# Kernel optimization log

Hardware: AMD Instinct MI355X
Metric: run time of the kernel (lower is better)

The kernel has to match this reference:

```python
import jax, jax.numpy as jnp
import numpy as np

HIDDEN = 1024
N_EMB = 4096
K_TOP = 64
EPS = 1e-6


def rmsnorm(x, w):
    xf = x.astype(jnp.float32)
    y = xf * jax.lax.rsqrt(jnp.mean(xf * xf, axis=-1, keepdims=True) + EPS)
    return y.astype(x.dtype) * w


def setup_inputs() -> dict:
    key = jax.random.key(0)
    ks = jax.random.split(key, 5)
    B, S, D, N = 16, 2048, HIDDEN, N_EMB
    bound = 1.0 / np.sqrt(D)  # torch Linear reset_parameters uniform bound
    return {
        "X": jax.random.normal(ks[0], (B, S, D), dtype=jnp.float32),
        "alpha": jnp.zeros((), dtype=jnp.float32),
        "E": jax.random.normal(ks[1], (N, D), dtype=jnp.float32) / np.sqrt(D),
        "Wq": jax.random.uniform(ks[2], (D, D), dtype=jnp.float32, minval=-bound, maxval=bound),
        "Wk": jax.random.uniform(ks[3], (D, D), dtype=jnp.float32, minval=-bound, maxval=bound),
        "xn_w": jnp.ones((D,), dtype=jnp.float32),
        "sn_w": jnp.ones((D,), dtype=jnp.float32),
        "on_w": jnp.ones((D,), dtype=jnp.float32),
    }


def reference(X, alpha, E, Wq, Wk, xn_w, sn_w, on_w):
    scale = HIDDEN ** (-0.5)
    Xn = rmsnorm(X, xn_w)            # (B,S,D)
    En = rmsnorm(E, sn_w)            # (N,D)
    Q = Xn @ Wq.T                    # (B,S,D)
    Km = En @ Wk.T                   # (N,D)
    scores = jnp.einsum('bsd,nd->bsn', Q, Km) * scale  # (B,S,N)
    global_scores = jnp.max(scores, axis=1)            # (B,N)
    top_vals, _ = jax.lax.top_k(global_scores, K_TOP)
    cutoff = top_vals[:, -1:]                          # (B,1)
    masked = jnp.where(global_scores >= cutoff, global_scores, -jnp.inf)
    dense_w = jax.nn.softmax(global_scores, axis=-1)
    sparse_w = jax.nn.softmax(masked, axis=-1)
    weights = alpha * dense_w + (1.0 - alpha) * sparse_w  # (B,N)
    O = rmsnorm(weights @ En, on_w)                      # (B,D)
    return O, weights
```

## Files before the change

### kernel.cpp

```cpp
#include <hip/hip_runtime.h>


namespace {

constexpr int D_DIM = 1024;
constexpr int NE    = 4096;
constexpr int BATCH = 16;
constexpr int SEQ   = 2048;
constexpr int MX    = BATCH * SEQ;
constexpr int KTOP  = 64;
constexpr int CAND  = 128;
constexpr int BK    = 32;

using f32x4  = __attribute__((ext_vector_type(4))) float;
using bf16x8 = __attribute__((ext_vector_type(8))) short;
using i32x4  = __attribute__((ext_vector_type(4))) int;

__device__ inline unsigned encf(float f) {
  unsigned u = __float_as_uint(f);
  return (u & 0x80000000u) ? ~u : (u | 0x80000000u);
}
__device__ inline float decf(unsigned e) {
  unsigned u = (e & 0x80000000u) ? (e ^ 0x80000000u) : ~e;
  return __uint_as_float(u);
}

__device__ inline unsigned short f2bf(float f) {
  unsigned u = __float_as_uint(f);
  unsigned lsb = (u >> 16) & 1u;
  u += 0x7fffu + lsb;
  return (unsigned short)(u >> 16);
}
__device__ inline float bf2f(unsigned short h) {
  return __uint_as_float(((unsigned)h) << 16);
}

__device__ inline void gload16(const void* gsrc, void* ldst) {
  __builtin_amdgcn_global_load_lds(
      (const __attribute__((address_space(1))) unsigned int*)gsrc,
      (__attribute__((address_space(3))) unsigned int*)ldst, 16, 0, 0);
}

#define LGK0_SB() do { asm volatile("s_waitcnt lgkmcnt(0)" ::: "memory"); \
                       __builtin_amdgcn_sched_barrier(0); } while (0)

__global__ void row_rinv_k(const float* __restrict__ X, float* __restrict__ rinv) {
  __shared__ float l4[4];
  int row = blockIdx.x;
  float4 v = ((const float4*)(X + (size_t)row * D_DIM))[threadIdx.x];
  float ss = v.x * v.x + v.y * v.y + v.z * v.z + v.w * v.w;
  for (int o = 32; o > 0; o >>= 1) ss += __shfl_xor(ss, o);
  int lane = threadIdx.x & 63, w = threadIdx.x >> 6;
  if (lane == 0) l4[w] = ss;
  __syncthreads();
  if (threadIdx.x == 0) {
    float t = l4[0] + l4[1] + l4[2] + l4[3];
    rinv[row] = rsqrtf(t * (1.0f / D_DIM) + 1e-6f);
  }
}

__global__ void rinv_quantx_k(const float* __restrict__ X, float* __restrict__ rinv,
                              float* __restrict__ sxr, int* __restrict__ XQ) {
  __shared__ float l4[4], m4[4];
  int row = blockIdx.x;
  float4 v = ((const float4*)(X + (size_t)row * D_DIM))[threadIdx.x];
  float ss = v.x * v.x + v.y * v.y + v.z * v.z + v.w * v.w;
  float am = fmaxf(fmaxf(fabsf(v.x), fabsf(v.y)), fmaxf(fabsf(v.z), fabsf(v.w)));
  for (int o = 32; o > 0; o >>= 1) {
    ss += __shfl_xor(ss, o);
    am = fmaxf(am, __shfl_xor(am, o));
  }
  int lane = threadIdx.x & 63, w = threadIdx.x >> 6;
  if (lane == 0) { l4[w] = ss; m4[w] = am; }
  __syncthreads();
  float t  = l4[0] + l4[1] + l4[2] + l4[3];
  float amax = fmaxf(fmaxf(m4[0], m4[1]), fmaxf(m4[2], m4[3]));
  amax = fmaxf(amax, 1e-30f);
  float ri = rsqrtf(t * (1.0f / D_DIM) + 1e-6f);
  if (threadIdx.x == 0) {
    rinv[row] = ri;
    sxr[row]  = ri * amax * (1.0f / 127.0f);
  }
  float qs = 127.0f / amax;
  int q0 = (int)rintf(v.x * qs) & 0xff;
  int q1 = (int)rintf(v.y * qs) & 0xff;
  int q2 = (int)rintf(v.z * qs) & 0xff;
  int q3 = (int)rintf(v.w * qs) & 0xff;
  XQ[(size_t)row * 256 + threadIdx.x] = q0 | (q1 << 8) | (q2 << 16) | (q3 << 24);
}

__global__ void quant_p_k(const unsigned short* __restrict__ PH,
                          const unsigned short* __restrict__ PL,
                          float* __restrict__ sp, int* __restrict__ PQ) {
  __shared__ float m4[4];
  int row = blockIdx.x;
  ushort4 h = *(const ushort4*)(PH + (size_t)row * D_DIM + threadIdx.x * 4);
  ushort4 l = *(const ushort4*)(PL + (size_t)row * D_DIM + threadIdx.x * 4);
  float p0 = bf2f(h.x) + bf2f(l.x);
  float p1 = bf2f(h.y) + bf2f(l.y);
  float p2 = bf2f(h.z) + bf2f(l.z);
  float p3 = bf2f(h.w) + bf2f(l.w);
  float am = fmaxf(fmaxf(fabsf(p0), fabsf(p1)), fmaxf(fabsf(p2), fabsf(p3)));
  for (int o = 32; o > 0; o >>= 1) am = fmaxf(am, __shfl_xor(am, o));
  int lane = threadIdx.x & 63, w = threadIdx.x >> 6;
  if (lane == 0) m4[w] = am;
  __syncthreads();
  float amax = fmaxf(fmaxf(m4[0], m4[1]), fmaxf(m4[2], m4[3]));
  amax = fmaxf(amax, 1e-30f);
  if (threadIdx.x == 0) sp[row] = amax * (1.0f / 127.0f);
  float qs = 127.0f / amax;
  int q0 = (int)rintf(p0 * qs) & 0xff;
  int q1 = (int)rintf(p1 * qs) & 0xff;
  int q2 = (int)rintf(p2 * qs) & 0xff;
  int q3 = (int)rintf(p3 * qs) & 0xff;
  PQ[(size_t)row * 256 + threadIdx.x] = q0 | (q1 << 8) | (q2 << 16) | (q3 << 24);
}

__global__ void prep_w_k(const float* __restrict__ Wq, const float* __restrict__ Wk,
                         const float* __restrict__ cw, float* __restrict__ T,
                         unsigned short* __restrict__ H, unsigned short* __restrict__ L) {
  __shared__ float t[32][33], u[32][33];
  int k0 = blockIdx.x * 32, d0 = blockIdx.y * 32;
  int tx = threadIdx.x & 31, ty4 = (threadIdx.x >> 5) * 4;
#pragma unroll
  for (int i = 0; i < 4; ++i) {
    t[ty4 + i][tx] = Wq[(size_t)(d0 + ty4 + i) * D_DIM + k0 + tx];
    u[ty4 + i][tx] = Wk[(size_t)(d0 + ty4 + i) * D_DIM + k0 + tx];
  }
  __syncthreads();
#pragma unroll
  for (int i = 0; i < 4; ++i) {
    int a = ty4 + i;
    T[(size_t)(k0 + a) * D_DIM + d0 + tx] = t[tx][a];
    float v = u[tx][a] * cw[k0 + a];
    unsigned short h = f2bf(v);
    H[(size_t)(k0 + a) * D_DIM + d0 + tx] = h;
    L[(size_t)(k0 + a) * D_DIM + d0 + tx] = f2bf(v - bf2f(h));
  }
}

template <int FPOUT>
__global__ __launch_bounds__(256, 2) void gemm_a32_k(
    const float* __restrict__ A, const float* __restrict__ rinv,
    const unsigned short* __restrict__ BH, const unsigned short* __restrict__ BL,
    unsigned short* __restrict__ OH, unsigned short* __restrict__ OL,
    float* __restrict__ Of) {
  __shared__ __align__(16) float lA[128 * 32];
  __shared__ __align__(16) unsigned short lBH[128 * 32];
  __shared__ __align__(16) unsigned short lBL[128 * 32];
  __shared__ float ldsR[128];

  int tid = threadIdx.x;
  int lane = tid & 63, wid = tid >> 6;
  int wr = wid >> 1, wc = wid & 1;
  int fr = lane & 15, fg = lane >> 4;
  long m0 = (long)blockIdx.x * 128;
  long n0 = (long)blockIdx.y * 128;

  if (tid < 128) ldsR[tid] = rinv ? rinv[m0 + tid] : 1.0f;

  f32x4 acc[4][4] = {};

  for (int kk = 0; kk < D_DIM; kk += BK) {
#pragma unroll
    for (int i = 0; i < 4; ++i) {
      int chunk = i * 256 + tid;
      int r = chunk >> 3, c = chunk & 7;
      int cs = c ^ (r & 7);
      const float* src = A + (m0 + r) * (long)D_DIM + kk + cs * 4;
      gload16(src, (void*)(lA + ((i * 256 + (tid & ~63)) << 2)));
    }
#pragma unroll
    for (int i = 0; i < 2; ++i) {
      int chunk = i * 256 + tid;
      int r = chunk >> 2, c = chunk & 3;
      int cs = c ^ ((r >> 1) & 3);
      long boff = (n0 + r) * (long)D_DIM + kk + cs * 8;
      int lo = (i * 256 + (tid & ~63)) << 3;
      gload16(BH + boff, (void*)(lBH + lo));
      gload16(BL + boff, (void*)(lBL + lo));
    }
    __syncthreads();

    bf16x8 aH[4], aL[4], bH[4], bL[4];
#pragma unroll
    for (int m = 0; m < 4; ++m) {
      int row = wr * 64 + m * 16 + fr;
      int rm = row & 7;
      f32x4 p0 = *(const f32x4*)(lA + row * 32 + (((fg * 2 + 0) ^ rm) * 4));
      f32x4 p1 = *(const f32x4*)(lA + row * 32 + (((fg * 2 + 1) ^ rm) * 4));
#pragma unroll
      for (int e = 0; e < 8; ++e) {
        float f = (e < 4) ? p0[e] : p1[e - 4];
        unsigned short h = f2bf(f);
        aH[m][e] = (short)h;
        aL[m][e] = (short)f2bf(f - bf2f(h));
      }
    }
#pragma unroll
    for (int n = 0; n < 4; ++n) {
      int row = wc * 64 + n * 16 + fr;
      int sc = fg ^ ((row >> 1) & 3);
      bH[n] = *(const bf16x8*)(lBH + row * 32 + sc * 8);
      bL[n] = *(const bf16x8*)(lBL + row * 32 + sc * 8);
    }
#pragma unroll
    for (int m = 0; m < 4; ++m)
#pragma unroll
      for (int n = 0; n < 4; ++n) {
        acc[m][n] = __builtin_amdgcn_mfma_f32_16x16x32_bf16(aH[m], bH[n], acc[m][n], 0, 0, 0);
        acc[m][n] = __builtin_amdgcn_mfma_f32_16x16x32_bf16(aH[m], bL[n], acc[m][n], 0, 0, 0);
        acc[m][n] = __builtin_amdgcn_mfma_f32_16x16x32_bf16(aL[m], bH[n], acc[m][n], 0, 0, 0);
      }
    __syncthreads();
  }

#pragma unroll
  for (int m = 0; m < 4; ++m) {
#pragma unroll
    for (int j = 0; j < 4; ++j) {
      int rloc = wr * 64 + m * 16 + fg * 4 + j;
      float rv = ldsR[rloc];
      long grow = m0 + rloc;
#pragma unroll
      for (int n = 0; n < 4; ++n) {
        long gcol = n0 + wc * 64 + n * 16 + fr;
        float v = acc[m][n][j] * rv;
        if (FPOUT) {
          Of[grow * D_DIM + gcol] = v;
        } else {
          unsigned short h = f2bf(v);
          OH[grow * D_DIM + gcol] = h;
          OL[grow * D_DIM + gcol] = f2bf(v - bf2f(h));
        }
      }
    }
  }
}

__global__ __launch_bounds__(512, 2) void gemm_scores1_k(
    const signed char* __restrict__ XQ, const signed char* __restrict__ PQ,
    const float* __restrict__ sxr, const float* __restrict__ sp,
    unsigned* __restrict__ gmax) {
  __shared__ __align__(16) signed char lA[2][256 * 64];
  __shared__ __align__(16) signed char lB[2][256 * 64];

  int tid = threadIdx.x;
  int lane = tid & 63, wid = tid >> 6;
  int wr = wid >> 2;
  int wcn = wid & 3;
  int fr = lane & 15, fg = lane >> 4;

  int id = blockIdx.x;
  int xcd = id & 7;
  int r = id >> 3;
  int tile_n = (r & 7) | ((r >> 7) << 3);
  int tile_m = xcd * 16 + ((r >> 3) & 15);
  long m0 = (long)tile_m * 256;
  long n0 = (long)tile_n * 256;

  auto stageTile = [&](int buf, int kt) {
    int kk = kt * 64;
#pragma unroll
    for (int i = 0; i < 2; ++i) {
      int chunk = i * 512 + tid;
      int r2 = chunk >> 2, c = chunk & 3;
      int cs = c ^ ((r2 >> 1) & 3);
      gload16(XQ + (m0 + r2) * (long)D_DIM + kk + cs * 16,
              (void*)(&lA[buf][0] + ((i * 512 + (tid & ~63)) << 4)));
    }
#pragma unroll
    for (int i = 0; i < 2; ++i) {
      int chunk = i * 512 + tid;
      int r2 = chunk >> 2, c = chunk & 3;
      int cs = c ^ ((r2 >> 1) & 3);
      gload16(PQ + (n0 + r2) * (long)D_DIM + kk + cs * 16,
              (void*)(&lB[buf][0] + ((i * 512 + (tid & ~63)) << 4)));
    }
  };

  i32x4 acc[8][4] = {};

  stageTile(0, 0);
  stageTile(1, 1);

  i32x4 aF[4], bF[4];

  for (int kt = 0; kt < 16; ++kt) {
    int cur = kt & 1;
    const signed char* As = &lA[cur][0];
    const signed char* Bs = &lB[cur][0];

    if (kt < 15) {
      asm volatile("s_waitcnt vmcnt(4)" ::: "memory");
    } else {
      asm volatile("s_waitcnt vmcnt(0)" ::: "memory");
    }
    __builtin_amdgcn_s_barrier();

#pragma unroll
    for (int mi = 0; mi < 4; ++mi) {
      int row = wr * 128 + mi * 16 + fr;
      int ck = fg ^ ((row >> 1) & 3);
      aF[mi] = *(const i32x4*)(As + row * 64 + ck * 16);
    }
#pragma unroll
    for (int ni = 0; ni < 2; ++ni) {
      int row = wcn * 64 + ni * 16 + fr;
      int ck = fg ^ ((row >> 1) & 3);
      bF[ni] = *(const i32x4*)(Bs + row * 64 + ck * 16);
    }
    LGK0_SB();
    __builtin_amdgcn_s_setprio(1);
#pragma unroll
    for (int mi = 0; mi < 4; ++mi)
#pragma unroll
      for (int ni = 0; ni < 2; ++ni)
        acc[mi][ni] = __builtin_amdgcn_mfma_i32_16x16x64_i8(
            aF[mi], bF[ni], acc[mi][ni], 0, 0, 0);
    __builtin_amdgcn_s_setprio(0);

#pragma unroll
    for (int ni = 2; ni < 4; ++ni) {
      int row = wcn * 64 + ni * 16 + fr;
      int ck = fg ^ ((row >> 1) & 3);
      bF[ni] = *(const i32x4*)(Bs + row * 64 + ck * 16);
    }
    LGK0_SB();
    __builtin_amdgcn_s_setprio(1);
#pragma unroll
    for (int mi = 0; mi < 4; ++mi)
#pragma unroll
      for (int ni = 2; ni < 4; ++ni)
        acc[mi][ni] = __builtin_amdgcn_mfma_i32_16x16x64_i8(
            aF[mi], bF[ni], acc[mi][ni], 0, 0, 0);
    __builtin_amdgcn_s_setprio(0);

#pragma unroll
    for (int mi = 0; mi < 4; ++mi) {
      int row = wr * 128 + (mi + 4) * 16 + fr;
      int ck = fg ^ ((row >> 1) & 3);
      aF[mi] = *(const i32x4*)(As + row * 64 + ck * 16);
    }
    LGK0_SB();
    __builtin_amdgcn_s_barrier();
    if (kt + 2 < 16) stageTile(cur, kt + 2);
    __builtin_amdgcn_s_setprio(1);
#pragma unroll
    for (int mi = 0; mi < 4; ++mi)
#pragma unroll
      for (int ni = 2; ni < 4; ++ni)
        acc[mi + 4][ni] = __builtin_amdgcn_mfma_i32_16x16x64_i8(
            aF[mi], bF[ni], acc[mi + 4][ni], 0, 0, 0);
    __builtin_amdgcn_s_setprio(0);

    __builtin_amdgcn_s_setprio(1);
#pragma unroll
    for (int mi = 0; mi < 4; ++mi)
#pragma unroll
      for (int ni = 0; ni < 2; ++ni)
        acc[mi + 4][ni] = __builtin_amdgcn_mfma_i32_16x16x64_i8(
            aF[mi], bF[ni], acc[mi + 4][ni], 0, 0, 0);
    __builtin_amdgcn_s_setprio(0);
  }

  int b = (int)(m0 >> 11);
#pragma unroll
  for (int ni = 0; ni < 4; ++ni) {
    long col = n0 + wcn * 64 + ni * 16 + fr;
    float spc = sp[col];
    float v = -3.0e38f;
#pragma unroll
    for (int mi = 0; mi < 8; ++mi) {
      const float* sr = sxr + m0 + wr * 128 + mi * 16 + fg * 4;
#pragma unroll
      for (int j = 0; j < 4; ++j)
        v = fmaxf(v, (float)acc[mi][ni][j] * sr[j]);
    }
    v *= spc;
    v = fmaxf(v, __shfl_xor(v, 16));
    v = fmaxf(v, __shfl_xor(v, 32));
    if (fg == 0) {
      atomicMax(&gmax[(long)b * NE + col], encf(v * 0.03125f));
    }
  }
}

__global__ void cand_select_k(const unsigned* __restrict__ gmax,
                              int* __restrict__ candIdx, unsigned* __restrict__ gmax2) {
  __shared__ unsigned enc[NE];
  __shared__ int ic[257];
  int tid = threadIdx.x;
  int lane = tid & 63, w = tid >> 6;
  int zb = blockIdx.x;
  if (tid < CAND) gmax2[zb * CAND + tid] = 0u;
  const unsigned* g = gmax + (size_t)zb * NE;
  for (int i = tid; i < NE; i += 256) enc[i] = g[i];
  __syncthreads();

  unsigned cur = 0;
  for (int bit = 31; bit >= 0; --bit) {
    unsigned cand = cur | (1u << bit);
    int c = 0;
    for (int i = tid; i < NE; i += 256) c += (enc[i] >= cand) ? 1 : 0;
    for (int o = 32; o > 0; o >>= 1) c += __shfl_xor(c, o);
    __syncthreads();
    if (lane == 0) ic[w] = c;
    __syncthreads();
    int tot = ic[0] + ic[1] + ic[2] + ic[3];
    if (tot >= CAND) cur = cand;
  }

  int myc = 0;
  for (int i = tid; i < NE; i += 256) myc += (enc[i] >= cur) ? 1 : 0;
  __syncthreads();
  ic[tid] = myc;
  __syncthreads();
  if (tid == 0) {
    int s = 0;
    for (int t = 0; t < 256; ++t) { int v = ic[t]; ic[t] = s; s += v; }
  }
  __syncthreads();
  int off = ic[tid];
  for (int i = tid; i < NE; i += 256)
    if (enc[i] >= cur) {
      if (off < CAND) candIdx[zb * CAND + off] = i;
      ++off;
    }
}

__global__ __launch_bounds__(256, 2) void gemm_rescore_k(
    const float* __restrict__ X, const float* __restrict__ rinvA,
    const unsigned short* __restrict__ PH, const unsigned short* __restrict__ PL,
    const int* __restrict__ candIdx, unsigned* __restrict__ gmax2) {
  __shared__ __align__(16) float lA[128 * 32];
  __shared__ __align__(16) unsigned short lBH[128 * 32], lBL[128 * 32];
  __shared__ float ldsR[128];

  int tid = threadIdx.x;
  int lane = tid & 63, wid = tid >> 6;
  int wr = wid >> 1, wc = wid & 1;
  int fr = lane & 15, fg = lane >> 4;
  int z = blockIdx.z;
  long m0 = (long)blockIdx.x * 128;
  long arow0 = (long)z * SEQ + m0;

  if (tid < 128) ldsR[tid] = rinvA[arow0 + tid];

  long bbase[2];
#pragma unroll
  for (int i = 0; i < 2; ++i) {
    int r = (i * 256 + tid) >> 2;
    bbase[i] = (long)candIdx[z * CAND + r] * D_DIM;
  }

  f32x4 acc[4][4] = {};

  for (int kk = 0; kk < D_DIM; kk += BK) {
#pragma unroll
    for (int i = 0; i < 4; ++i) {
      int chunk = i * 256 + tid;
      int r = chunk >> 3, c = chunk & 7;
      int cs = c ^ (r & 7);
      const float* src = X + (arow0 + r) * (long)D_DIM + kk + cs * 4;
      gload16(src, (void*)(lA + ((i * 256 + (tid & ~63)) << 2)));
    }
#pragma unroll
    for (int i = 0; i < 2; ++i) {
      int chunk = i * 256 + tid;
      int c = chunk & 3;
      int r = chunk >> 2;
      int cs = c ^ ((r >> 1) & 3);
      long boff = bbase[i] + kk + cs * 8;
      int lo = (i * 256 + (tid & ~63)) << 3;
      gload16(PH + boff, (void*)(lBH + lo));
      gload16(PL + boff, (void*)(lBL + lo));
    }
    __syncthreads();

    bf16x8 aH[4], aL[4], bH[4], bL[4];
#pragma unroll
    for (int m = 0; m < 4; ++m) {
      int row = wr * 64 + m * 16 + fr;
      int rm = row & 7;
      f32x4 p0 = *(const f32x4*)(lA + row * 32 + (((fg * 2 + 0) ^ rm) * 4));
      f32x4 p1 = *(const f32x4*)(lA + row * 32 + (((fg * 2 + 1) ^ rm) * 4));
#pragma unroll
      for (int e = 0; e < 8; ++e) {
        float f = (e < 4) ? p0[e] : p1[e - 4];
        unsigned short h = f2bf(f);
        aH[m][e] = (short)h;
        aL[m][e] = (short)f2bf(f - bf2f(h));
      }
    }
#pragma unroll
    for (int n = 0; n < 4; ++n) {
      int row = wc * 64 + n * 16 + fr;
      int sc = fg ^ ((row >> 1) & 3);
      bH[n] = *(const bf16x8*)(lBH + row * 32 + sc * 8);
      bL[n] = *(const bf16x8*)(lBL + row * 32 + sc * 8);
    }
#pragma unroll
    for (int m = 0; m < 4; ++m)
#pragma unroll
      for (int n = 0; n < 4; ++n) {
        acc[m][n] = __builtin_amdgcn_mfma_f32_16x16x32_bf16(aH[m], bH[n], acc[m][n], 0, 0, 0);
        acc[m][n] = __builtin_amdgcn_mfma_f32_16x16x32_bf16(aH[m], bL[n], acc[m][n], 0, 0, 0);
        acc[m][n] = __builtin_amdgcn_mfma_f32_16x16x32_bf16(aL[m], bH[n], acc[m][n], 0, 0, 0);
      }
    __syncthreads();
  }

#pragma unroll
  for (int n = 0; n < 4; ++n) {
    float v = -3.0e38f;
#pragma unroll
    for (int m = 0; m < 4; ++m)
#pragma unroll
      for (int j = 0; j < 4; ++j) {
        float rv = ldsR[wr * 64 + m * 16 + fg * 4 + j];
        v = fmaxf(v, acc[m][n][j] * rv);
      }
    v = fmaxf(v, __shfl_xor(v, 16));
    v = fmaxf(v, __shfl_xor(v, 32));
    if (fg == 0) {
      int col = wc * 64 + n * 16 + fr;
      atomicMax(&gmax2[z * CAND + col], encf(v * 0.03125f));
    }
  }
}

__global__ void final_k(const unsigned* __restrict__ gmax,
                        const unsigned* __restrict__ gmax2,
                        const int* __restrict__ candIdx,
                        const float* __restrict__ alpha_p,
                        const float* __restrict__ E, const float* __restrict__ rinvE,
                        const float* __restrict__ sn_w, const float* __restrict__ on_w,
                        float* __restrict__ wout, float* __restrict__ O) {
  __shared__ unsigned enc[NE];
  __shared__ int sel[NE];
  __shared__ unsigned ubc[4];
  __shared__ float l4[4];
  __shared__ int ic[257];
  int tid = threadIdx.x;
  int lane = tid & 63, w = tid >> 6;
  int b = blockIdx.x;
  const unsigned* g = gmax + (size_t)b * NE;
  for (int i = tid; i < NE; i += 256) enc[i] = g[i];
  __syncthreads();
  if (tid < CAND) enc[candIdx[b * CAND + tid]] = gmax2[b * CAND + tid];
  __syncthreads();

  unsigned mx = 0;
  for (int i = tid; i < NE; i += 256) mx = enc[i] > mx ? enc[i] : mx;
  for (int o = 32; o > 0; o >>= 1) {
    unsigned other = (unsigned)__shfl_xor((int)mx, o);
    if (other > mx) mx = other;
  }
  if (lane == 0) ubc[w] = mx;
  __syncthreads();
  unsigned m1e = ubc[0];
  for (int t = 1; t < 4; ++t) m1e = ubc[t] > m1e ? ubc[t] : m1e;
  float m1 = decf(m1e);

  unsigned cur = 0;
  for (int bit = 31; bit >= 0; --bit) {
    unsigned cand = cur | (1u << bit);
    int c = 0;
    for (int i = tid; i < NE; i += 256) c += (enc[i] >= cand) ? 1 : 0;
    for (int o = 32; o > 0; o >>= 1) c += __shfl_xor(c, o);
    __syncthreads();
    if (lane == 0) ic[w] = c;
    __syncthreads();
    int tot = ic[0] + ic[1] + ic[2] + ic[3];
    if (tot >= KTOP) cur = cand;
  }

  float sd = 0.f, ssum = 0.f;
  for (int i = tid; i < NE; i += 256) {
    float e = expf(decf(enc[i]) - m1);
    sd += e;
    if (enc[i] >= cur) ssum += e;
  }
  for (int o = 32; o > 0; o >>= 1) { sd += __shfl_xor(sd, o); ssum += __shfl_xor(ssum, o); }
  __syncthreads();
  if (lane == 0) { l4[w] = sd; }
  __syncthreads();
  float SD = l4[0] + l4[1] + l4[2] + l4[3];
  __syncthreads();
  if (lane == 0) { l4[w] = ssum; }
  __syncthreads();
  float SS = l4[0] + l4[1] + l4[2] + l4[3];

  float alpha = alpha_p[0];
  float wd = alpha / SD;
  float ws_ = (1.0f - alpha) / SS;
  for (int i = tid; i < NE; i += 256) {
    float e = expf(decf(enc[i]) - m1);
    float wv = wd * e + ((enc[i] >= cur) ? ws_ * e : 0.0f);
    wout[(size_t)b * NE + i] = wv;
  }

  int myc = 0;
  for (int i = tid; i < NE; i += 256) myc += (enc[i] >= cur) ? 1 : 0;
  __syncthreads();
  ic[tid] = myc;
  __syncthreads();
  if (tid == 0) {
    int s = 0;
    for (int t = 0; t < 256; ++t) { int v = ic[t]; ic[t] = s; s += v; }
    ic[256] = s;
  }
  __syncthreads();
  int off = ic[tid];
  for (int i = tid; i < NE; i += 256)
    if (enc[i] >= cur) sel[off++] = i;
  __syncthreads();
  int nsel = ic[256];

  float acc[4] = {0.f, 0.f, 0.f, 0.f};
  if (alpha == 0.0f) {
    float coef = wd + ws_;
    for (int j = 0; j < nsel; ++j) {
      int n = sel[j];
      float e = expf(decf(enc[n]) - m1);
      float wv = coef * e * rinvE[n];
      const float* er = E + (size_t)n * D_DIM;
#pragma unroll
      for (int i = 0; i < 4; ++i) acc[i] += wv * er[tid + 256 * i];
    }
  } else {
    for (int n = 0; n < NE; ++n) {
      float e = expf(decf(enc[n]) - m1);
      float wv = (wd * e + ((enc[n] >= cur) ? ws_ * e : 0.0f)) * rinvE[n];
      const float* er = E + (size_t)n * D_DIM;
#pragma unroll
      for (int i = 0; i < 4; ++i) acc[i] += wv * er[tid + 256 * i];
    }
  }
  float ssq = 0.f;
#pragma unroll
  for (int i = 0; i < 4; ++i) {
    acc[i] *= sn_w[tid + 256 * i];
    ssq += acc[i] * acc[i];
  }
  for (int o = 32; o > 0; o >>= 1) ssq += __shfl_xor(ssq, o);
  if (lane == 0) l4[w] = ssq;
  __syncthreads();
  float tot = l4[0] + l4[1] + l4[2] + l4[3];
  float rn = rsqrtf(tot * (1.0f / D_DIM) + 1e-6f);
#pragma unroll
  for (int i = 0; i < 4; ++i)
    O[(size_t)b * D_DIM + tid + 256 * i] = acc[i] * rn * on_w[tid + 256 * i];
}

}

extern "C" void kernel_launch(void* const* d_in, const int* in_sizes, int n_in,
                              void* d_out, int out_size, void* d_ws, size_t ws_size,
                              hipStream_t stream) {
  const float* X     = (const float*)d_in[0];
  const float* alpha = (const float*)d_in[1];
  const float* E     = (const float*)d_in[2];
  const float* Wq    = (const float*)d_in[3];
  const float* Wk    = (const float*)d_in[4];
  const float* xn_w  = (const float*)d_in[5];
  const float* sn_w  = (const float*)d_in[6];
  const float* on_w  = (const float*)d_in[7];
  float* O    = (float*)d_out;
  float* Wout = (float*)d_out + (size_t)BATCH * D_DIM;

  char* ws = (char*)d_ws;
  size_t off = 0;
  auto alloc = [&](size_t bytes) {
    char* p = ws + off;
    off += (bytes + 255) & ~(size_t)255;
    return p;
  };
  signed char*    XQ    = (signed char*)alloc((size_t)MX * D_DIM);
  signed char*    PQ    = (signed char*)alloc((size_t)NE * D_DIM);
  float*          WqTf  = (float*)alloc((size_t)D_DIM * D_DIM * 4);
  unsigned short* WkTH  = (unsigned short*)alloc((size_t)D_DIM * D_DIM * 2);
  unsigned short* WkTL  = (unsigned short*)alloc((size_t)D_DIM * D_DIM * 2);
  unsigned short* W2TH  = (unsigned short*)alloc((size_t)D_DIM * D_DIM * 2);
  unsigned short* W2TL  = (unsigned short*)alloc((size_t)D_DIM * D_DIM * 2);
  unsigned short* PH    = (unsigned short*)alloc((size_t)NE * D_DIM * 2);
  unsigned short* PL    = (unsigned short*)alloc((size_t)NE * D_DIM * 2);
  float* rinvX = (float*)alloc((size_t)MX * 4);
  float* sxr   = (float*)alloc((size_t)MX * 4);
  float* rinvE = (float*)alloc((size_t)NE * 4);
  float* sp    = (float*)alloc((size_t)NE * 4);
  unsigned* gmax  = (unsigned*)alloc((size_t)BATCH * NE * 4);
  unsigned* gmax2 = (unsigned*)alloc((size_t)BATCH * CAND * 4);
  int* candIdx = (int*)alloc((size_t)BATCH * CAND * 4);
  if (off > ws_size) return;

  hipMemsetAsync(gmax, 0, (size_t)BATCH * NE * 4, stream);

  row_rinv_k<<<NE, 256, 0, stream>>>(E, rinvE);
  prep_w_k<<<dim3(D_DIM / 32, D_DIM / 32), 256, 0, stream>>>(
      Wq, Wk, sn_w, WqTf, WkTH, WkTL);
  gemm_a32_k<0><<<dim3(8, 8), 256, 0, stream>>>(
      WqTf, xn_w, WkTH, WkTL, W2TH, W2TL, nullptr);
  gemm_a32_k<0><<<dim3(NE / 128, D_DIM / 128), 256, 0, stream>>>(
      E, rinvE, W2TH, W2TL, PH, PL, nullptr);
  quant_p_k<<<NE, 256, 0, stream>>>(PH, PL, sp, (int*)PQ);

  rinv_quantx_k<<<MX, 256, 0, stream>>>(X, rinvX, sxr, (int*)XQ);
  gemm_scores1_k<<<(MX / 256) * (NE / 256), 512, 0, stream>>>(XQ, PQ, sxr, sp, gmax);

  cand_select_k<<<BATCH, 256, 0, stream>>>(gmax, candIdx, gmax2);
  gemm_rescore_k<<<dim3(SEQ / 128, 1, BATCH), 256, 0, stream>>>(
      X, rinvX, PH, PL, candIdx, gmax2);
  final_k<<<BATCH, 256, 0, stream>>>(gmax, gmax2, candIdx, alpha, E, rinvE,
                                     sn_w, on_w, Wout, O);
}
```

Before: 428.7 us.

## Halve M tile of int8 score GEMM to 128 rows and raise occupancy

The int8 score GEMM now uses a 128x256 block tile instead of 256x256, with each wave computing a 64x64 sub-tile (acc 4x4 instead of 8x4). Launch bounds go from 2 to 4 blocks per CU, the grid doubles, and the per-row scales are cached in LDS for the max epilogue. The prefetch of the next K tile moves earlier in the loop. The aim is more resident waves for latency hiding and fewer registers per thread, in exchange for less operand reuse and more global traffic on the B operand.

New measurement: 427.3 us. No clear change (-0.3%).

```diff
diff --git a/kernel.cpp b/kernel.cpp
--- a/kernel.cpp
+++ b/kernel.cpp
@@ -238,36 +238,37 @@
   }
 }
 
-__global__ __launch_bounds__(512, 2) void gemm_scores1_k(
+__global__ __launch_bounds__(512, 4) void gemm_scores1_k(
     const signed char* __restrict__ XQ, const signed char* __restrict__ PQ,
     const float* __restrict__ sxr, const float* __restrict__ sp,
     unsigned* __restrict__ gmax) {
-  __shared__ __align__(16) signed char lA[2][256 * 64];
+  __shared__ __align__(16) signed char lA[2][128 * 64];
   __shared__ __align__(16) signed char lB[2][256 * 64];
+  __shared__ float ldsR[128];
 
   int tid = threadIdx.x;
   int lane = tid & 63, wid = tid >> 6;
-  int wr = wid >> 2;
-  int wcn = wid & 3;
+  int wwr = wid >> 2;
+  int wwc = wid & 3;
   int fr = lane & 15, fg = lane >> 4;
 
   int id = blockIdx.x;
   int xcd = id & 7;
   int r = id >> 3;
-  int tile_n = (r & 7) | ((r >> 7) << 3);
-  int tile_m = xcd * 16 + ((r >> 3) & 15);
-  long m0 = (long)tile_m * 256;
+  int tile_n = (r & 7) | ((r >> 8) << 3);
+  int tile_m = xcd * 32 + ((r >> 3) & 31);
+  long m0 = (long)tile_m * 128;
   long n0 = (long)tile_n * 256;
+
+  if (tid < 128) ldsR[tid] = sxr[m0 + tid];
 
   auto stageTile = [&](int buf, int kt) {
     int kk = kt * 64;
-#pragma unroll
-    for (int i = 0; i < 2; ++i) {
-      int chunk = i * 512 + tid;
-      int r2 = chunk >> 2, c = chunk & 3;
+    {
+      int r2 = tid >> 2, c = tid & 3;
       int cs = c ^ ((r2 >> 1) & 3);
       gload16(XQ + (m0 + r2) * (long)D_DIM + kk + cs * 16,
-              (void*)(&lA[buf][0] + ((i * 512 + (tid & ~63)) << 4)));
+              (void*)(&lA[buf][0] + ((tid & ~63) << 4)));
     }
 #pragma unroll
     for (int i = 0; i < 2; ++i) {
@@ -279,10 +280,11 @@
     }
   };
 
-  i32x4 acc[8][4] = {};
+  i32x4 acc[4][4] = {};
 
   stageTile(0, 0);
   stageTile(1, 1);
+  asm volatile("s_waitcnt lgkmcnt(0)" ::: "memory");
 
   i32x4 aF[4], bF[4];
 
@@ -292,7 +294,7 @@
     const signed char* Bs = &lB[cur][0];
 
     if (kt < 15) {
-      asm volatile("s_waitcnt vmcnt(4)" ::: "memory");
+      asm volatile("s_waitcnt vmcnt(3)" ::: "memory");
     } else {
       asm volatile("s_waitcnt vmcnt(0)" ::: "memory");
     }
@@ -300,13 +302,13 @@
 
 #pragma unroll
     for (int mi = 0; mi < 4; ++mi) {
-      int row = wr * 128 + mi * 16 + fr;
+      int row = wwr * 64 + mi * 16 + fr;
       int ck = fg ^ ((row >> 1) & 3);
       aF[mi] = *(const i32x4*)(As + row * 64 + ck * 16);
     }
 #pragma unroll
     for (int ni = 0; ni < 2; ++ni) {
-      int row = wcn * 64 + ni * 16 + fr;
+      int row = wwc * 64 + ni * 16 + fr;
       int ck = fg ^ ((row >> 1) & 3);
       bF[ni] = *(const i32x4*)(Bs + row * 64 + ck * 16);
     }
@@ -322,11 +324,13 @@
 
 #pragma unroll
     for (int ni = 2; ni < 4; ++ni) {
-      int row = wcn * 64 + ni * 16 + fr;
+      int row = wwc * 64 + ni * 16 + fr;
       int ck = fg ^ ((row >> 1) & 3);
       bF[ni] = *(const i32x4*)(Bs + row * 64 + ck * 16);
     }
     LGK0_SB();
+    __builtin_amdgcn_s_barrier();
+    if (kt + 2 < 16) stageTile(cur, kt + 2);
     __builtin_amdgcn_s_setprio(1);
 #pragma unroll
     for (int mi = 0; mi < 4; ++mi)
@@ -335,48 +339,21 @@
         acc[mi][ni] = __builtin_amdgcn_mfma_i32_16x16x64_i8(
             aF[mi], bF[ni], acc[mi][ni], 0, 0, 0);
     __builtin_amdgcn_s_setprio(0);
-
-#pragma unroll
-    for (int mi = 0; mi < 4; ++mi) {
-      int row = wr * 128 + (mi + 4) * 16 + fr;
-      int ck = fg ^ ((row >> 1) & 3);
-      aF[mi] = *(const i32x4*)(As + row * 64 + ck * 16);
-    }
-    LGK0_SB();
-    __builtin_amdgcn_s_barrier();
-    if (kt + 2 < 16) stageTile(cur, kt + 2);
-    __builtin_amdgcn_s_setprio(1);
-#pragma unroll
-    for (int mi = 0; mi < 4; ++mi)
-#pragma unroll
-      for (int ni = 2; ni < 4; ++ni)
-        acc[mi + 4][ni] = __builtin_amdgcn_mfma_i32_16x16x64_i8(
-            aF[mi], bF[ni], acc[mi + 4][ni], 0, 0, 0);
-    __builtin_amdgcn_s_setprio(0);
-
-    __builtin_amdgcn_s_setprio(1);
-#pragma unroll
-    for (int mi = 0; mi < 4; ++mi)
-#pragma unroll
-      for (int ni = 0; ni < 2; ++ni)
-        acc[mi + 4][ni] = __builtin_amdgcn_mfma_i32_16x16x64_i8(
-            aF[mi], bF[ni], acc[mi + 4][ni], 0, 0, 0);
-    __builtin_amdgcn_s_setprio(0);
   }
 
   int b = (int)(m0 >> 11);
 #pragma unroll
   for (int ni = 0; ni < 4; ++ni) {
-    long col = n0 + wcn * 64 + ni * 16 + fr;
+    long col = n0 + wwc * 64 + ni * 16 + fr;
     float spc = sp[col];
     float v = -3.0e38f;
 #pragma unroll
-    for (int mi = 0; mi < 8; ++mi) {
-      const float* sr = sxr + m0 + wr * 128 + mi * 16 + fg * 4;
-#pragma unroll
-      for (int j = 0; j < 4; ++j)
-        v = fmaxf(v, (float)acc[mi][ni][j] * sr[j]);
-    }
+    for (int mi = 0; mi < 4; ++mi)
+#pragma unroll
+      for (int j = 0; j < 4; ++j) {
+        int row = wwr * 64 + mi * 16 + fg * 4 + j;
+        v = fmaxf(v, (float)acc[mi][ni][j] * ldsR[row]);
+      }
     v *= spc;
     v = fmaxf(v, __shfl_xor(v, 16));
     v = fmaxf(v, __shfl_xor(v, 32));
@@ -707,7 +684,7 @@
   quant_p_k<<<NE, 256, 0, stream>>>(PH, PL, sp, (int*)PQ);
 
   rinv_quantx_k<<<MX, 256, 0, stream>>>(X, rinvX, sxr, (int*)XQ);
-  gemm_scores1_k<<<(MX / 256) * (NE / 256), 512, 0, stream>>>(XQ, PQ, sxr, sp, gmax);
+  gemm_scores1_k<<<(MX / 128) * (NE / 256), 512, 0, stream>>>(XQ, PQ, sxr, sp, gmax);
 
   cand_select_k<<<BATCH, 256, 0, stream>>>(gmax, candIdx, gmax2);
   gemm_rescore_k<<<dim3(SEQ / 128, 1, BATCH), 256, 0, stream>>>(
```
